# Kernel optimization log

Measured on AMD Instinct MI355X. Metric: run time of the kernel, lower is better.

## Reference

```python
import jax, jax.numpy as jnp
import numpy as np

B, T, C = 2, 2048, 1024
N_HEAD = 16
HEAD_DIM = C // N_HEAD


def setup_inputs() -> dict:
    key = jax.random.key(0)
    k1, k2, k3 = jax.random.split(key, 3)
    x = jax.random.normal(k1, (B, T, C), dtype=jnp.float32)
    # broadcastable causal mask: 1 where attendable, 0 where masked
    mask = jnp.tril(jnp.ones((T, T), dtype=jnp.int32))[None, None, :, :]
    W_qkv = jax.random.normal(k2, (C, 3 * C), dtype=jnp.float32) * (1.0 / np.sqrt(C))
    b_qkv = jnp.zeros((3 * C,), dtype=jnp.float32)
    W_out = jax.random.normal(k3, (C, C), dtype=jnp.float32) * (1.0 / np.sqrt(C))
    b_out = jnp.zeros((C,), dtype=jnp.float32)
    return {"x": x, "mask": mask, "W_qkv": W_qkv, "b_qkv": b_qkv, "W_out": W_out, "b_out": b_out}


def reference(x, mask, W_qkv, b_qkv, W_out, b_out):
    Bx, Tx, Cx = x.shape
    # fused QKV projection
    qkv = x @ W_qkv + b_qkv  # [B, T, 3C]
    qkv = qkv.reshape(Bx, Tx, 3, N_HEAD, HEAD_DIM).transpose(2, 0, 3, 1, 4)  # [3, B, H, T, D]
    q, k, v = qkv[0], qkv[1], qkv[2]
    scale = 1.0 / jnp.sqrt(jnp.asarray(HEAD_DIM, dtype=x.dtype))
    att = jnp.einsum('bhqd,bhkd->bhqk', q, k) * scale  # [B, H, T, T]
    att = jnp.where(mask == 0, -jnp.inf, att)
    att = jax.nn.softmax(att, axis=-1)
    # dropout is deterministic=True in the original -> identity
    y = jnp.einsum('bhqk,bhkd->bhqd', att, v)  # [B, H, T, D]
    y = y.transpose(0, 2, 1, 3).reshape(Bx, Tx, Cx)
    return y @ W_out + b_out
```

## Files before the change

kernel.cpp:

```cpp
#include <hip/hip_runtime.h>
#include <hip/hip_bf16.h>
#include <math.h>

#define B_  2
#define T_  2048
#define C_  1024
#define NH  16
#define HD  64

typedef __attribute__((ext_vector_type(8))) short short8;
typedef __attribute__((ext_vector_type(4))) float f32x4;

__device__ __forceinline__ void gload_lds16(const void* g, void* l) {
    __builtin_amdgcn_global_load_lds(
        (const __attribute__((address_space(1))) void*)g,
        (__attribute__((address_space(3))) void*)l, 16, 0, 0);
}

__device__ __forceinline__ unsigned short f2bf(float f) {
    __hip_bfloat16 b = __float2bfloat16(f);
    return *reinterpret_cast<unsigned short*>(&b);
}

__global__ __launch_bounds__(256) void cast_bf16_kernel(
    const float* __restrict__ in, __hip_bfloat16* __restrict__ out, int n4)
{
    const int i = blockIdx.x * 256 + threadIdx.x;
    if (i >= n4) return;
    const float4 v = reinterpret_cast<const float4*>(in)[i];
    ushort4 o;
    o.x = f2bf(v.x); o.y = f2bf(v.y); o.z = f2bf(v.z); o.w = f2bf(v.w);
    reinterpret_cast<ushort4*>(out)[i] = o;
}

__global__ __launch_bounds__(256) void transpose_cast_kernel(
    const float* __restrict__ W, __hip_bfloat16* __restrict__ Wt, int R, int Ccols)
{
    __shared__ float tile[32][33];
    const int c0 = blockIdx.x * 32, r0 = blockIdx.y * 32;
    const int tx = threadIdx.x & 31, ty = threadIdx.x >> 5;
    #pragma unroll
    for (int i = 0; i < 32; i += 8)
        tile[ty + i][tx] = W[(size_t)(r0 + ty + i) * Ccols + c0 + tx];
    __syncthreads();
    #pragma unroll
    for (int i = 0; i < 32; i += 8)
        Wt[(size_t)(c0 + ty + i) * R + r0 + tx] = __float2bfloat16(tile[tx][ty + i]);
}

#define GBM 128
#define GBN 128
#define GBK 64

__global__ __launch_bounds__(256) void gemm_bf16_mfma(
    const __hip_bfloat16* __restrict__ A,
    const __hip_bfloat16* __restrict__ Bt,
    const float* __restrict__ bias,
    float* __restrict__ Cf,
    __hip_bfloat16* __restrict__ Cb,
    __hip_bfloat16* __restrict__ vt,
    int M, int N, int K)
{
    __shared__ __align__(16) __hip_bfloat16 As[GBM * GBK];
    __shared__ __align__(16) __hip_bfloat16 Bs[GBN * GBK];

    const int tid = threadIdx.x;
    const int lane = tid & 63;
    const int wid = tid >> 6;
    const int wr = wid >> 1, wc = wid & 1;
    const int lr = lane & 15;
    const int lk = (lane >> 4) * 8;

    const size_t rowA0 = (size_t)blockIdx.y * GBM;
    const size_t colB0 = (size_t)blockIdx.x * GBN;

    f32x4 acc[4][4];
    #pragma unroll
    for (int i = 0; i < 4; ++i)
        #pragma unroll
        for (int j = 0; j < 4; ++j)
            acc[i][j] = (f32x4){0.f, 0.f, 0.f, 0.f};

    for (int k0 = 0; k0 < K; k0 += GBK) {
        #pragma unroll
        for (int it = 0; it < 4; ++it) {
            const int idx = tid + it * 256;
            const int r  = idx >> 3;
            const int kc = (idx & 7) * 8;
            gload_lds16(A  + (rowA0 + r) * K + k0 + kc, &As[idx * 8]);
            gload_lds16(Bt + (colB0 + r) * K + k0 + kc, &Bs[idx * 8]);
        }
        __syncthreads();

        #pragma unroll
        for (int kk = 0; kk < GBK; kk += 32) {
            short8 af[4], bf[4];
            #pragma unroll
            for (int i = 0; i < 4; ++i)
                af[i] = *reinterpret_cast<const short8*>(
                    &As[(wr * 64 + i * 16 + lr) * GBK + kk + lk]);
            #pragma unroll
            for (int j = 0; j < 4; ++j)
                bf[j] = *reinterpret_cast<const short8*>(
                    &Bs[(wc * 64 + j * 16 + lr) * GBK + kk + lk]);
            #pragma unroll
            for (int i = 0; i < 4; ++i)
                #pragma unroll
                for (int j = 0; j < 4; ++j)
                    acc[i][j] = __builtin_amdgcn_mfma_f32_16x16x32_bf16(
                        af[i], bf[j], acc[i][j], 0, 0, 0);
        }
        __syncthreads();
    }

    const int orow = (lane >> 4) * 4;
    #pragma unroll
    for (int i = 0; i < 4; ++i) {
        #pragma unroll
        for (int j = 0; j < 4; ++j) {
            const size_t col = colB0 + wc * 64 + j * 16 + lr;
            const float bb = bias[col];
            float v[4];
            #pragma unroll
            for (int r = 0; r < 4; ++r) v[r] = acc[i][j][r] + bb;
            const size_t row0 = rowA0 + wr * 64 + i * 16 + orow;
            if (Cf) {
                #pragma unroll
                for (int r = 0; r < 4; ++r)
                    Cf[(row0 + r) * N + col] = v[r];
            } else {
                #pragma unroll
                for (int r = 0; r < 4; ++r)
                    Cb[(row0 + r) * N + col] = __float2bfloat16(v[r]);
            }
            if (vt && (int)col >= 2 * C_) {
                const int vc = (int)col - 2 * C_;
                const int hh = vc >> 6, dd = vc & 63;
                const int bb_ = (int)(row0 >> 11);
                const int t0  = (int)(row0 & 2047);
                ushort4 o;
                o.x = f2bf(v[0]); o.y = f2bf(v[1]); o.z = f2bf(v[2]); o.w = f2bf(v[3]);
                *reinterpret_cast<ushort4*>(
                    vt + (((size_t)(bb_ * NH + hh) * 64 + dd) * T_ + t0)) = o;
            }
        }
    }
}

__global__ __launch_bounds__(256) void attn_mfma_kernel(
    const __hip_bfloat16* __restrict__ qkvb,
    const __hip_bfloat16* __restrict__ vtg,
    __hip_bfloat16* __restrict__ yb)
{
    const int bh = blockIdx.x;
    const int b = bh >> 4, h = bh & 15;
    const int qt = (int)gridDim.y - 1 - (int)blockIdx.y;
    const int tid = threadIdx.x;
    const int w = tid >> 6, lane = tid & 63;
    const int lr = lane & 15, lg = lane >> 4;

    __shared__ __align__(16) __hip_bfloat16 Ks[64 * 64];
    __shared__ __align__(16) __hip_bfloat16 Vts[64 * 64];
    __shared__ __align__(16) __hip_bfloat16 Pl[4][16 * 64];

    const int q0 = qt * 64;
    const int qrow = q0 + w * 16;
    const size_t s3C = 3 * C_;

    const __hip_bfloat16* qp =
        qkvb + ((size_t)(b * T_) + qrow + lr) * s3C + h * 64 + lg * 8;
    const short8 qf0 = *reinterpret_cast<const short8*>(qp);
    const short8 qf1 = *reinterpret_cast<const short8*>(qp + 32);

    f32x4 o_acc[4];
    #pragma unroll
    for (int db = 0; db < 4; ++db) o_acc[db] = (f32x4){0.f, 0.f, 0.f, 0.f};
    float m_r[4] = {-INFINITY, -INFINITY, -INFINITY, -INFINITY};
    float l_r[4] = {0.f, 0.f, 0.f, 0.f};

    char* KsB  = (char*)Ks;
    char* VtsB = (char*)Vts;
    char* PlB  = (char*)Pl[w];

    for (int t = 0; t <= qt; ++t) {
        __syncthreads();
        #pragma unroll
        for (int rr = 0; rr < 2; ++rr) {
            const int slot = (rr * 4 + w) * 64 + lane;
            const int row = slot >> 3;
            const int gblk = (slot & 7) ^ (row & 7);
            gload_lds16(qkvb + ((size_t)(b * T_) + t * 64 + row) * s3C
                             + C_ + h * 64 + gblk * 8,
                        KsB + slot * 16);
            gload_lds16(vtg + ((size_t)bh * 64 + row) * T_ + t * 64 + gblk * 8,
                        VtsB + slot * 16);
        }
        __syncthreads();

        f32x4 sacc[4];
        #pragma unroll
        for (int kb = 0; kb < 4; ++kb) sacc[kb] = (f32x4){0.f, 0.f, 0.f, 0.f};
        #pragma unroll
        for (int kb = 0; kb < 4; ++kb) {
            const int key = kb * 16 + lr;
            const short8 kf0 = *reinterpret_cast<const short8*>(
                KsB + key * 128 + ((lg) ^ (key & 7)) * 16);
            const short8 kf1 = *reinterpret_cast<const short8*>(
                KsB + key * 128 + ((4 + lg) ^ (key & 7)) * 16);
            sacc[kb] = __builtin_amdgcn_mfma_f32_16x16x32_bf16(qf0, kf0, sacc[kb], 0, 0, 0);
            sacc[kb] = __builtin_amdgcn_mfma_f32_16x16x32_bf16(qf1, kf1, sacc[kb], 0, 0, 0);
        }

        #pragma unroll
        for (int r = 0; r < 4; ++r) {
            const int qg = qrow + lg * 4 + r;
            const int qlocal = lg * 4 + r;
            float sv[4];
            float vmax = -INFINITY;
            #pragma unroll
            for (int kb = 0; kb < 4; ++kb) {
                const int keyg = t * 64 + kb * 16 + lr;
                float s = sacc[kb][r] * 0.125f;
                s = (keyg <= qg) ? s : -INFINITY;
                sv[kb] = s;
                vmax = fmaxf(vmax, s);
            }
            vmax = fmaxf(vmax, __shfl_xor(vmax, 1));
            vmax = fmaxf(vmax, __shfl_xor(vmax, 2));
            vmax = fmaxf(vmax, __shfl_xor(vmax, 4));
            vmax = fmaxf(vmax, __shfl_xor(vmax, 8));
            const float mnew = fmaxf(m_r[r], vmax);
            const float corr = __expf(m_r[r] - mnew);
            m_r[r] = mnew;
            float psum = 0.f;
            #pragma unroll
            for (int kb = 0; kb < 4; ++kb) {
                const float p = __expf(sv[kb] - mnew);
                psum += p;
                const int key = kb * 16 + lr;
                const int byte = qlocal * 128
                               + (((key >> 3) ^ (qlocal & 7)) * 16) + (key & 7) * 2;
                *reinterpret_cast<__hip_bfloat16*>(PlB + byte) = __float2bfloat16(p);
            }
            psum += __shfl_xor(psum, 1);
            psum += __shfl_xor(psum, 2);
            psum += __shfl_xor(psum, 4);
            psum += __shfl_xor(psum, 8);
            l_r[r] = l_r[r] * corr + psum;
            #pragma unroll
            for (int db = 0; db < 4; ++db) {
                o_acc[db][0 + r] *= corr;
            }
        }

        const short8 pf0 = *reinterpret_cast<const short8*>(
            PlB + lr * 128 + ((lg) ^ (lr & 7)) * 16);
        const short8 pf1 = *reinterpret_cast<const short8*>(
            PlB + lr * 128 + ((4 + lg) ^ (lr & 7)) * 16);
        #pragma unroll
        for (int db = 0; db < 4; ++db) {
            const int dd = db * 16 + lr;
            const short8 vf0 = *reinterpret_cast<const short8*>(
                VtsB + dd * 128 + ((lg) ^ (dd & 7)) * 16);
            const short8 vf1 = *reinterpret_cast<const short8*>(
                VtsB + dd * 128 + ((4 + lg) ^ (dd & 7)) * 16);
            o_acc[db] = __builtin_amdgcn_mfma_f32_16x16x32_bf16(pf0, vf0, o_acc[db], 0, 0, 0);
            o_acc[db] = __builtin_amdgcn_mfma_f32_16x16x32_bf16(pf1, vf1, o_acc[db], 0, 0, 0);
        }
    }

    #pragma unroll
    for (int r = 0; r < 4; ++r) {
        const float inv = 1.f / l_r[r];
        const int qg = qrow + lg * 4 + r;
        __hip_bfloat16* yp = yb + ((size_t)(b * T_) + qg) * C_ + h * 64;
        #pragma unroll
        for (int db = 0; db < 4; ++db)
            yp[db * 16 + lr] = __float2bfloat16(o_acc[db][r] * inv);
    }
}

extern "C" void kernel_launch(void* const* d_in, const int* in_sizes, int n_in,
                              void* d_out, int out_size, void* d_ws, size_t ws_size,
                              hipStream_t stream)
{
    const float* x     = (const float*)d_in[0];
    const float* W_qkv = (const float*)d_in[2];
    const float* b_qkv = (const float*)d_in[3];
    const float* W_out = (const float*)d_in[4];
    const float* b_out = (const float*)d_in[5];
    float* out = (float*)d_out;

    __hip_bfloat16* qkvb = (__hip_bfloat16*)d_ws;
    __hip_bfloat16* vtg  = qkvb + (size_t)B_ * T_ * 3 * C_;
    __hip_bfloat16* xb   = vtg  + (size_t)B_ * NH * 64 * T_;
    __hip_bfloat16* wqt  = xb   + (size_t)B_ * T_ * C_;
    __hip_bfloat16* wot  = wqt  + (size_t)3 * C_ * C_;
    __hip_bfloat16* yb   = wot  + (size_t)C_ * C_;

    const int M = B_ * T_;

    cast_bf16_kernel<<<(M * C_ / 4 + 255) / 256, 256, 0, stream>>>(x, xb, M * C_ / 4);
    {
        dim3 g(3 * C_ / 32, C_ / 32);
        transpose_cast_kernel<<<g, 256, 0, stream>>>(W_qkv, wqt, C_, 3 * C_);
    }
    {
        dim3 g(C_ / 32, C_ / 32);
        transpose_cast_kernel<<<g, 256, 0, stream>>>(W_out, wot, C_, C_);
    }

    {
        dim3 grid(3 * C_ / GBN, M / GBM);
        gemm_bf16_mfma<<<grid, 256, 0, stream>>>(xb, wqt, b_qkv,
                                                 nullptr, qkvb, vtg,
                                                 M, 3 * C_, C_);
    }
    {
        dim3 grid(B_ * NH, T_ / 64);
        attn_mfma_kernel<<<grid, 256, 0, stream>>>(qkvb, vtg, yb);
    }
    {
        dim3 grid(C_ / GBN, M / GBM);
        gemm_bf16_mfma<<<grid, 256, 0, stream>>>(yb, wot, b_out,
                                                 out, nullptr, nullptr,
                                                 M, C_, C_);
    }
}
```

Measured before the change: 239.9 us.

## Double-buffer K/V tiles and streamline online softmax in attention kernel

The attention kernel now double-buffers the K and V^T LDS tiles, issuing the async global-to-LDS load for the next tile before computing on the current one, with one barrier per iteration. It folds the softmax scale and log2(e) into Q so it can use exp2f, applies the causal mask only on the diagonal tile, and rescales the running max only when it grows by more than 4. The row sum comes from an extra MFMA against a ones column instead of shuffle reductions, and s_setprio hints surround the MFMA blocks. These changes cost more LDS and one extra MFMA per tile, and the lazy rescale and bf16-rounded probabilities add small numerical risk.

```diff
diff --git a/kernel.cpp b/kernel.cpp
--- a/kernel.cpp
+++ b/kernel.cpp
@@ -159,31 +159,38 @@
     const int w = tid >> 6, lane = tid & 63;
     const int lr = lane & 15, lg = lane >> 4;
 
-    __shared__ __align__(16) __hip_bfloat16 Ks[64 * 64];
-    __shared__ __align__(16) __hip_bfloat16 Vts[64 * 64];
+    __shared__ __align__(16) __hip_bfloat16 Ks[2][64 * 64];
+    __shared__ __align__(16) __hip_bfloat16 Vts[2][64 * 64];
     __shared__ __align__(16) __hip_bfloat16 Pl[4][16 * 64];
 
-    const int q0 = qt * 64;
-    const int qrow = q0 + w * 16;
+    const int qrow = qt * 64 + w * 16;
     const size_t s3C = 3 * C_;
 
+    const float qscale = 0.125f * 1.44269504f;
     const __hip_bfloat16* qp =
         qkvb + ((size_t)(b * T_) + qrow + lr) * s3C + h * 64 + lg * 8;
-    const short8 qf0 = *reinterpret_cast<const short8*>(qp);
-    const short8 qf1 = *reinterpret_cast<const short8*>(qp + 32);
-
-    f32x4 o_acc[4];
-    #pragma unroll
-    for (int db = 0; db < 4; ++db) o_acc[db] = (f32x4){0.f, 0.f, 0.f, 0.f};
+    short8 qf0 = *reinterpret_cast<const short8*>(qp);
+    short8 qf1 = *reinterpret_cast<const short8*>(qp + 32);
+    #pragma unroll
+    for (int j = 0; j < 8; ++j) {
+        const float f0 = __uint_as_float(((unsigned)(unsigned short)qf0[j]) << 16);
+        const float f1 = __uint_as_float(((unsigned)(unsigned short)qf1[j]) << 16);
+        qf0[j] = (short)f2bf(f0 * qscale);
+        qf1[j] = (short)f2bf(f1 * qscale);
+    }
+
+    short8 vone;
+    #pragma unroll
+    for (int j = 0; j < 8; ++j) vone[j] = (lr == 0) ? (short)0x3F80 : (short)0;
+
+    f32x4 o_acc[5];
+    #pragma unroll
+    for (int db = 0; db < 5; ++db) o_acc[db] = (f32x4){0.f, 0.f, 0.f, 0.f};
     float m_r[4] = {-INFINITY, -INFINITY, -INFINITY, -INFINITY};
-    float l_r[4] = {0.f, 0.f, 0.f, 0.f};
-
-    char* KsB  = (char*)Ks;
-    char* VtsB = (char*)Vts;
-    char* PlB  = (char*)Pl[w];
-
-    for (int t = 0; t <= qt; ++t) {
-        __syncthreads();
+
+    char* PlB = (char*)Pl[w];
+
+    auto STAGE = [&](int t, int bi) {
         #pragma unroll
         for (int rr = 0; rr < 2; ++rr) {
             const int slot = (rr * 4 + w) * 64 + lane;
@@ -191,15 +198,26 @@
             const int gblk = (slot & 7) ^ (row & 7);
             gload_lds16(qkvb + ((size_t)(b * T_) + t * 64 + row) * s3C
                              + C_ + h * 64 + gblk * 8,
-                        KsB + slot * 16);
+                        (char*)Ks[bi] + slot * 16);
             gload_lds16(vtg + ((size_t)bh * 64 + row) * T_ + t * 64 + gblk * 8,
-                        VtsB + slot * 16);
-        }
-        __syncthreads();
+                        (char*)Vts[bi] + slot * 16);
+        }
+    };
+
+    STAGE(0, 0);
+    __syncthreads();
+    int buf = 0;
+
+    for (int t = 0; t <= qt; ++t) {
+        if (t < qt) STAGE(t + 1, buf ^ 1);
+
+        const char* KsB  = (const char*)Ks[buf];
+        const char* VtsB = (const char*)Vts[buf];
 
         f32x4 sacc[4];
         #pragma unroll
         for (int kb = 0; kb < 4; ++kb) sacc[kb] = (f32x4){0.f, 0.f, 0.f, 0.f};
+        __builtin_amdgcn_s_setprio(1);
         #pragma unroll
         for (int kb = 0; kb < 4; ++kb) {
             const int key = kb * 16 + lr;
@@ -210,53 +228,52 @@
             sacc[kb] = __builtin_amdgcn_mfma_f32_16x16x32_bf16(qf0, kf0, sacc[kb], 0, 0, 0);
             sacc[kb] = __builtin_amdgcn_mfma_f32_16x16x32_bf16(qf1, kf1, sacc[kb], 0, 0, 0);
         }
-
+        __builtin_amdgcn_s_setprio(0);
+
+        const bool diag = (t == qt);
         #pragma unroll
         for (int r = 0; r < 4; ++r) {
-            const int qg = qrow + lg * 4 + r;
             const int qlocal = lg * 4 + r;
             float sv[4];
-            float vmax = -INFINITY;
-            #pragma unroll
-            for (int kb = 0; kb < 4; ++kb) {
-                const int keyg = t * 64 + kb * 16 + lr;
-                float s = sacc[kb][r] * 0.125f;
-                s = (keyg <= qg) ? s : -INFINITY;
-                sv[kb] = s;
-                vmax = fmaxf(vmax, s);
-            }
+            if (diag) {
+                const int qg = qrow + qlocal;
+                #pragma unroll
+                for (int kb = 0; kb < 4; ++kb) {
+                    const int keyg = t * 64 + kb * 16 + lr;
+                    sv[kb] = (keyg <= qg) ? sacc[kb][r] : -INFINITY;
+                }
+            } else {
+                #pragma unroll
+                for (int kb = 0; kb < 4; ++kb) sv[kb] = sacc[kb][r];
+            }
+            float vmax = fmaxf(fmaxf(sv[0], sv[1]), fmaxf(sv[2], sv[3]));
             vmax = fmaxf(vmax, __shfl_xor(vmax, 1));
             vmax = fmaxf(vmax, __shfl_xor(vmax, 2));
             vmax = fmaxf(vmax, __shfl_xor(vmax, 4));
             vmax = fmaxf(vmax, __shfl_xor(vmax, 8));
-            const float mnew = fmaxf(m_r[r], vmax);
-            const float corr = __expf(m_r[r] - mnew);
-            m_r[r] = mnew;
-            float psum = 0.f;
+
+            if (vmax > m_r[r] + 4.f) {
+                const float corr = exp2f(m_r[r] - vmax);
+                m_r[r] = vmax;
+                #pragma unroll
+                for (int db = 0; db < 5; ++db) o_acc[db][r] *= corr;
+            }
+            const float mm = m_r[r];
             #pragma unroll
             for (int kb = 0; kb < 4; ++kb) {
-                const float p = __expf(sv[kb] - mnew);
-                psum += p;
+                const float p = exp2f(sv[kb] - mm);
                 const int key = kb * 16 + lr;
                 const int byte = qlocal * 128
                                + (((key >> 3) ^ (qlocal & 7)) * 16) + (key & 7) * 2;
                 *reinterpret_cast<__hip_bfloat16*>(PlB + byte) = __float2bfloat16(p);
             }
-            psum += __shfl_xor(psum, 1);
-            psum += __shfl_xor(psum, 2);
-            psum += __shfl_xor(psum, 4);
-            psum += __shfl_xor(psum, 8);
-            l_r[r] = l_r[r] * corr + psum;
-            #pragma unroll
-            for (int db = 0; db < 4; ++db) {
-                o_acc[db][0 + r] *= corr;
-            }
         }
 
         const short8 pf0 = *reinterpret_cast<const short8*>(
             PlB + lr * 128 + ((lg) ^ (lr & 7)) * 16);
         const short8 pf1 = *reinterpret_cast<const short8*>(
             PlB + lr * 128 + ((4 + lg) ^ (lr & 7)) * 16);
+        __builtin_amdgcn_s_setprio(1);
         #pragma unroll
         for (int db = 0; db < 4; ++db) {
             const int dd = db * 16 + lr;
@@ -267,11 +284,18 @@
             o_acc[db] = __builtin_amdgcn_mfma_f32_16x16x32_bf16(pf0, vf0, o_acc[db], 0, 0, 0);
             o_acc[db] = __builtin_amdgcn_mfma_f32_16x16x32_bf16(pf1, vf1, o_acc[db], 0, 0, 0);
         }
+        o_acc[4] = __builtin_amdgcn_mfma_f32_16x16x32_bf16(pf0, vone, o_acc[4], 0, 0, 0);
+        o_acc[4] = __builtin_amdgcn_mfma_f32_16x16x32_bf16(pf1, vone, o_acc[4], 0, 0, 0);
+        __builtin_amdgcn_s_setprio(0);
+
+        __syncthreads();
+        buf ^= 1;
     }
 
     #pragma unroll
     for (int r = 0; r < 4; ++r) {
-        const float inv = 1.f / l_r[r];
+        const float lsum = __shfl(o_acc[4][r], (lane & 48));
+        const float inv = 1.f / lsum;
         const int qg = qrow + lg * 4 + r;
         __hip_bfloat16* yp = yb + ((size_t)(b * T_) + qg) * C_ + h * 64;
         #pragma unroll
```

After: 244.5 us. No clear change (+1.9%).
